# Performance work log

Measured on AMD Instinct MI355X. Metric: run time of the kernel, lower is better.

## Reference

```python
import jax, jax.numpy as jnp
import numpy as np
from jax import lax

ORDER = 2  # diffusion order per support, as in __init__(order=2)


def setup_inputs() -> dict:
    key = jax.random.key(0)
    k1, k2, k3 = jax.random.split(key, 3)
    N, C, V, L = 64, 32, 512, 13
    S, Kt, C_out = 3, 3, 32
    C_cat = (ORDER * S + 1) * C  # 224
    x = jax.random.normal(k1, (N, C, V, L), dtype=jnp.float32)
    support = jax.random.uniform(k2, (S, V, V), dtype=jnp.float32)
    # Conv2d(c_in=224, c_out=32, kernel=(1,Kt)) weights, PyTorch OIHW layout
    W = jax.random.normal(k3, (C_out, C_cat, 1, Kt), dtype=jnp.float32) * 0.02
    b = jnp.zeros((C_out,), dtype=jnp.float32)
    return {"x": x, "support": support, "W": W, "b": b}


def _nconv(x, A):
    # torch: A = A.T; einsum('ncvl,vw->ncwl', x, A.T)
    # => out[n,c,w,l] = sum_v A[w,v] * x[n,c,v,l]
    return jnp.einsum('ncvl,wv->ncwl', x, A)


def reference(x, support, W, b):
    out = [x]
    for s in range(support.shape[0]):  # small fixed support_len=3
        A = support[s]
        x1 = _nconv(x, A)
        out.append(x1)
        for _ in range(2, ORDER + 1):
            x1 = _nconv(x1, A)
            out.append(x1)
    h = jnp.concatenate(out, axis=1)  # [N, (order*S+1)*C, V, L]
    # Conv2d kernel (1, Kt), no padding, stride 1 -> temporal conv
    y = lax.conv_general_dilated(
        h, W, window_strides=(1, 1), padding='VALID',
        dimension_numbers=('NCHW', 'OIHW', 'NCHW'))
    y = y + b[None, :, None, None]
    # dropout is identity in eval mode
    return y
```

## Files before the change

### kernel.cpp

```cpp
#include <hip/hip_runtime.h>

typedef __attribute__((ext_vector_type(4))) float f32x4;
typedef __attribute__((ext_vector_type(8))) __bf16 bf16x8;
typedef __attribute__((ext_vector_type(4))) __bf16 bf16x4;
typedef __attribute__((ext_vector_type(4))) int i32x4;

#define SXE (26624 * 512)

__global__ __launch_bounds__(256)
void prep_x(const float* __restrict__ x, __bf16* __restrict__ Xv2) {
  const int vt = blockIdx.x, n = blockIdx.y, tid = threadIdx.x;
  __shared__ float Xs[32 * 209];
  const float* src = x + ((size_t)n * 32) * 6656 + vt * 16 * 13;
  for (int i = tid; i < 32 * 208; i += 256) {
    const int c = i / 208, r = i - c * 208;
    Xs[c * 209 + r] = src[(size_t)c * 6656 + r];
  }
  __syncthreads();
  for (int j = tid; j < 416; j += 256) {
    const int c = j & 31, l = j >> 5;
    bf16x8 o8[2];
    #pragma unroll
    for (int v = 0; v < 16; ++v) o8[v >> 3][v & 7] = (__bf16)Xs[c * 209 + v * 13 + l];
    __bf16* d = Xv2 + (((size_t)n * 13 + l) * 32 + c) * 512 + vt * 16;
    *(bf16x8*)d = o8[0];
    *(bf16x8*)(d + 8) = o8[1];
  }
}

__global__ __launch_bounds__(256)
void cast_A(const float* __restrict__ A, __bf16* __restrict__ Ab) {
  const int i = blockIdx.x * 256 + threadIdx.x;
  const float4 f = ((const float4*)A)[i];
  bf16x4 o;
  o[0] = (__bf16)f.x; o[1] = (__bf16)f.y; o[2] = (__bf16)f.z; o[3] = (__bf16)f.w;
  ((bf16x4*)Ab)[i] = o;
}

__global__ __launch_bounds__(256)
void gemm_bf16(const __bf16* __restrict__ Ab, const __bf16* __restrict__ SRC,
               __bf16* __restrict__ DSTB, size_t srcStride, size_t dstStride) {
  const int tid = threadIdx.x;
  const int lane = tid & 63, wave = tid >> 6, q = lane >> 4;
  const int bx = blockIdx.x, by = blockIdx.y, s = blockIdx.z;

  const __bf16* Amat = Ab + (size_t)s * 512 * 512;
  const __bf16* B = SRC + (size_t)s * srcStride;
  __bf16* D = DSTB + (size_t)s * dstStride;

  const int W0 = by * 128, B0 = bx * 128;
  const int wm = wave >> 1, wn = wave & 1;

  __shared__ __bf16 As[128 * 64];
  __shared__ __bf16 Bs[128 * 64];

  f32x4 acc[4][4];
  #pragma unroll
  for (int m = 0; m < 4; ++m)
    #pragma unroll
    for (int n = 0; n < 4; ++n) acc[m][n] = {0.f, 0.f, 0.f, 0.f};

  const int srow = lane >> 3, spos = lane & 7;

  for (int kt = 0; kt < 8; ++kt) {
    const int k0 = kt * 64;
    #pragma unroll
    for (int i = 0; i < 4; ++i) {
      const int slot = i * 4 + wave;
      const int r = slot * 8 + srow;
      const int gc = spos ^ (r & 7);
      const __bf16* ga = Amat + (size_t)(W0 + r) * 512 + k0 + gc * 8;
      const __bf16* gb = B    + (size_t)(B0 + r) * 512 + k0 + gc * 8;
      char* la = (char*)As + slot * 1024 + lane * 16;
      char* lb = (char*)Bs + slot * 1024 + lane * 16;
      __builtin_amdgcn_global_load_lds((const __attribute__((address_space(1))) unsigned int*)ga,
                                       (__attribute__((address_space(3))) unsigned int*)la, 16, 0, 0);
      __builtin_amdgcn_global_load_lds((const __attribute__((address_space(1))) unsigned int*)gb,
                                       (__attribute__((address_space(3))) unsigned int*)lb, 16, 0, 0);
    }
    __syncthreads();
    #pragma unroll
    for (int ks = 0; ks < 2; ++ks) {
      bf16x8 af[4], df[4];
      const int ch = ks * 4 + q;
      #pragma unroll
      for (int m = 0; m < 4; ++m) {
        const int r = wm * 64 + m * 16 + (lane & 15);
        af[m] = *(const bf16x8*)((const char*)As + r * 128 + ((ch ^ (r & 7)) << 4));
      }
      #pragma unroll
      for (int n = 0; n < 4; ++n) {
        const int r = wn * 64 + n * 16 + (lane & 15);
        df[n] = *(const bf16x8*)((const char*)Bs + r * 128 + ((ch ^ (r & 7)) << 4));
      }
      #pragma unroll
      for (int m = 0; m < 4; ++m)
        #pragma unroll
        for (int n = 0; n < 4; ++n)
          acc[m][n] = __builtin_amdgcn_mfma_f32_16x16x32_bf16(af[m], df[n], acc[m][n], 0, 0, 0);
    }
    __syncthreads();
  }

  #pragma unroll
  for (int m = 0; m < 4; ++m) {
    const int w = W0 + wm * 64 + m * 16 + q * 4;
    #pragma unroll
    for (int n = 0; n < 4; ++n) {
      const int b = B0 + wn * 64 + n * 16 + (lane & 15);
      bf16x4 o4;
      o4[0] = (__bf16)acc[m][n][0]; o4[1] = (__bf16)acc[m][n][1];
      o4[2] = (__bf16)acc[m][n][2]; o4[3] = (__bf16)acc[m][n][3];
      *(bf16x4*)(D + (size_t)b * 512 + w) = o4;
    }
  }
}

__global__ __launch_bounds__(256)
void conv_kernel(const __bf16* __restrict__ Xv2, const __bf16* __restrict__ Y1,
                 const __bf16* __restrict__ Y2, const float* __restrict__ W,
                 const float* __restrict__ bias, float* __restrict__ y) {
  const int vt = blockIdx.x;
  const int n  = blockIdx.y;
  const int tid = threadIdx.x;
  const int lane = tid & 63, wave = tid >> 6, q = lane >> 4, r16 = lane & 15;

  __shared__ char sm[59392];
  char* Ws = sm + 53248;

  const __bf16* gsrc[7] = {Xv2, Y1, Y2, Y1 + (size_t)SXE, Y2 + (size_t)SXE,
                           Y1 + 2 * (size_t)SXE, Y2 + 2 * (size_t)SXE};

  f32x4 acc[11][2];
  #pragma unroll
  for (int t = 0; t < 11; ++t) { acc[t][0] = {0,0,0,0}; acc[t][1] = {0,0,0,0}; }

  for (int g = 0; g < 7; ++g) {
    __syncthreads();
    const __bf16* src = gsrc[g] + ((size_t)n * 416) * 512 + vt * 64;
    #pragma unroll
    for (int it = 0; it < 13; ++it) {
      const int idx = it * 256 + tid;
      const int l = idx >> 8, rem = idx & 255, c = rem >> 3, h = rem & 7;
      i32x4 val = *(const i32x4*)(src + ((size_t)(l * 32 + c) << 9) + h * 8);
      *(i32x4*)(sm + l * 4096 + c * 128 + h * 16) = val;
    }
    for (int idx = tid; idx < 768; idx += 256) {
      const int f = idx >> 7, rem2 = idx & 127, lw = rem2 >> 1, half = rem2 & 1;
      const int kt = f >> 1, of = f & 1;
      const int o = of * 16 + (lw & 15);
      const int cc = g * 32 + (lw >> 4) * 8 + half * 4;
      bf16x4 w4;
      #pragma unroll
      for (int j = 0; j < 4; ++j)
        w4[j] = (__bf16)W[((size_t)o * 224 + cc + j) * 3 + kt];
      *(bf16x4*)(Ws + idx * 8) = w4;
    }
    __syncthreads();

    bf16x8 a8[13];
    const int gbase = q * 8 * 128 + (wave * 16 + r16) * 2;
    #pragma unroll
    for (int l = 0; l < 13; ++l) {
      bf16x8 a;
      #pragma unroll
      for (int j = 0; j < 8; ++j)
        a[j] = *(const __bf16*)(sm + l * 4096 + gbase + j * 128);
      a8[l] = a;
    }
    bf16x8 wf[6];
    #pragma unroll
    for (int f = 0; f < 6; ++f)
      wf[f] = *(const bf16x8*)(Ws + (f * 64 + lane) * 16);

    #pragma unroll
    for (int kt = 0; kt < 3; ++kt)
      #pragma unroll
      for (int of = 0; of < 2; ++of)
        #pragma unroll
        for (int t = 0; t < 11; ++t)
          acc[t][of] = __builtin_amdgcn_mfma_f32_16x16x32_bf16(a8[t + kt], wf[kt * 2 + of], acc[t][of], 0, 0, 0);
  }

  float* Ds = (float*)sm;
  const int o16 = lane & 15;
  for (int p = 0; p < 2; ++p) {
    __syncthreads();
    #pragma unroll
    for (int t = 0; t < 11; ++t) {
      const int vbase = wave * 16 + q * 4;
      #pragma unroll
      for (int rg = 0; rg < 4; ++rg)
        Ds[o16 * 708 + (vbase + rg) * 11 + t] = acc[t][p][rg];
    }
    __syncthreads();
    for (int i = 0; i < 11; ++i) {
      const int cg = tid + i * 256;
      const int oo = cg / 176, ch = cg - oo * 176;
      f32x4 v4 = *(const f32x4*)(Ds + oo * 708 + ch * 4);
      const float bo = bias[p * 16 + oo];
      v4[0] += bo; v4[1] += bo; v4[2] += bo; v4[3] += bo;
      float* yp = y + (((size_t)n * 32 + p * 16 + oo) * 512 + vt * 64) * 11 + ch * 4;
      *(f32x4*)yp = v4;
    }
  }
}

extern "C" void kernel_launch(void* const* d_in, const int* in_sizes, int n_in,
                              void* d_out, int out_size, void* d_ws, size_t ws_size,
                              hipStream_t stream) {
  (void)in_sizes; (void)n_in; (void)out_size; (void)ws_size;
  const float* x = (const float*)d_in[0];
  const float* A = (const float*)d_in[1];
  const float* W = (const float*)d_in[2];
  const float* b = (const float*)d_in[3];
  float* y = (float*)d_out;

  char* ws = (char*)d_ws;
  const size_t SXB = (size_t)SXE * 2;
  __bf16* Xv2 = (__bf16*)ws;
  __bf16* Y1  = (__bf16*)(ws + SXB);
  __bf16* Y2  = (__bf16*)(ws + 4 * SXB);
  __bf16* Ab  = (__bf16*)(ws + 7 * SXB);

  cast_A<<<dim3(768), 256, 0, stream>>>(A, Ab);
  prep_x<<<dim3(32, 64), 256, 0, stream>>>(x, Xv2);
  gemm_bf16<<<dim3(208, 4, 3), 256, 0, stream>>>(Ab, Xv2, Y1, 0, (size_t)SXE);
  gemm_bf16<<<dim3(208, 4, 3), 256, 0, stream>>>(Ab, Y1, Y2, (size_t)SXE, (size_t)SXE);
  conv_kernel<<<dim3(8, 64), 256, 0, stream>>>(Xv2, Y1, Y2, W, b, y);
}
```

Baseline: 235.6 us.

## Widen GEMM tile to 256x128 and remap blocks for XCD-aware locality

The diffusion GEMM tile grows from 128x128 to 256 rows of A by 128 columns, so each wave holds a 4x8 accumulator array and every B tile loaded from global memory is reused twice as much. The launch becomes a flat 1D grid with a block index remap that spreads consecutive logical tiles across the 8 XCDs, so tiles sharing the same B columns and support land on the same XCD and can share its L2. The change raises register pressure and LDS use to 48KB, which may lower occupancy, and halves the block count.

```diff
diff --git a/kernel.cpp b/kernel.cpp
--- a/kernel.cpp
+++ b/kernel.cpp
@@ -39,75 +39,80 @@
 
 __global__ __launch_bounds__(256)
 void gemm_bf16(const __bf16* __restrict__ Ab, const __bf16* __restrict__ SRC,
-               __bf16* __restrict__ DSTB, size_t srcStride, size_t dstStride) {
+               __bf16* __restrict__ DSTB, size_t srcStride, size_t dstStride, int cpx) {
   const int tid = threadIdx.x;
-  const int lane = tid & 63, wave = tid >> 6, q = lane >> 4;
-  const int bx = blockIdx.x, by = blockIdx.y, s = blockIdx.z;
+  const int lane = tid & 63, wave = tid >> 6, q = lane >> 4, r16 = lane & 15;
+
+  const int bid = blockIdx.x;
+  const int lg = (bid & 7) * cpx + (bid >> 3);
+  const int bx = lg / 6, r6 = lg % 6, s = r6 >> 1, by = r6 & 1;
 
   const __bf16* Amat = Ab + (size_t)s * 512 * 512;
   const __bf16* B = SRC + (size_t)s * srcStride;
   __bf16* D = DSTB + (size_t)s * dstStride;
 
-  const int W0 = by * 128, B0 = bx * 128;
+  const int W0 = by * 256, B0 = bx * 128;
   const int wm = wave >> 1, wn = wave & 1;
 
-  __shared__ __bf16 As[128 * 64];
-  __shared__ __bf16 Bs[128 * 64];
-
-  f32x4 acc[4][4];
+  __shared__ char gsm[49152];
+  char* As = gsm;
+  char* Bs = gsm + 32768;
+
+  f32x4 acc[4][8];
   #pragma unroll
   for (int m = 0; m < 4; ++m)
     #pragma unroll
-    for (int n = 0; n < 4; ++n) acc[m][n] = {0.f, 0.f, 0.f, 0.f};
+    for (int n = 0; n < 8; ++n) acc[m][n] = {0.f, 0.f, 0.f, 0.f};
 
   const int srow = lane >> 3, spos = lane & 7;
 
   for (int kt = 0; kt < 8; ++kt) {
     const int k0 = kt * 64;
     #pragma unroll
-    for (int i = 0; i < 4; ++i) {
+    for (int i = 0; i < 12; ++i) {
       const int slot = i * 4 + wave;
-      const int r = slot * 8 + srow;
-      const int gc = spos ^ (r & 7);
-      const __bf16* ga = Amat + (size_t)(W0 + r) * 512 + k0 + gc * 8;
-      const __bf16* gb = B    + (size_t)(B0 + r) * 512 + k0 + gc * 8;
-      char* la = (char*)As + slot * 1024 + lane * 16;
-      char* lb = (char*)Bs + slot * 1024 + lane * 16;
-      __builtin_amdgcn_global_load_lds((const __attribute__((address_space(1))) unsigned int*)ga,
-                                       (__attribute__((address_space(3))) unsigned int*)la, 16, 0, 0);
-      __builtin_amdgcn_global_load_lds((const __attribute__((address_space(1))) unsigned int*)gb,
-                                       (__attribute__((address_space(3))) unsigned int*)lb, 16, 0, 0);
+      const int rr = (slot & 31 & ~32) ;
+      (void)rr;
+      const int gc = spos ^ (((slot & 31) * 0 + (slot < 32 ? (slot * 8 + srow) : ((slot - 32) * 8 + srow))) & 7);
+      const int row = (slot < 32) ? (slot * 8 + srow) : ((slot - 32) * 8 + srow);
+      const __bf16* g = (slot < 32)
+          ? Amat + (size_t)(W0 + row) * 512 + k0 + ((spos ^ (row & 7)) * 8)
+          : B    + (size_t)(B0 + row) * 512 + k0 + ((spos ^ (row & 7)) * 8);
+      (void)gc;
+      char* ld = gsm + slot * 1024 + lane * 16;
+      __builtin_amdgcn_global_load_lds((const __attribute__((address_space(1))) unsigned int*)g,
+                                       (__attribute__((address_space(3))) unsigned int*)ld, 16, 0, 0);
     }
     __syncthreads();
     #pragma unroll
     for (int ks = 0; ks < 2; ++ks) {
-      bf16x8 af[4], df[4];
+      bf16x8 af[8], df[4];
       const int ch = ks * 4 + q;
       #pragma unroll
+      for (int n = 0; n < 8; ++n) {
+        const int r = wn * 128 + n * 16 + r16;
+        af[n] = *(const bf16x8*)(As + r * 128 + ((ch ^ (r & 7)) << 4));
+      }
+      #pragma unroll
       for (int m = 0; m < 4; ++m) {
-        const int r = wm * 64 + m * 16 + (lane & 15);
-        af[m] = *(const bf16x8*)((const char*)As + r * 128 + ((ch ^ (r & 7)) << 4));
-      }
-      #pragma unroll
-      for (int n = 0; n < 4; ++n) {
-        const int r = wn * 64 + n * 16 + (lane & 15);
-        df[n] = *(const bf16x8*)((const char*)Bs + r * 128 + ((ch ^ (r & 7)) << 4));
+        const int r = wm * 64 + m * 16 + r16;
+        df[m] = *(const bf16x8*)(Bs + r * 128 + ((ch ^ (r & 7)) << 4));
       }
       #pragma unroll
       for (int m = 0; m < 4; ++m)
         #pragma unroll
-        for (int n = 0; n < 4; ++n)
-          acc[m][n] = __builtin_amdgcn_mfma_f32_16x16x32_bf16(af[m], df[n], acc[m][n], 0, 0, 0);
+        for (int n = 0; n < 8; ++n)
+          acc[m][n] = __builtin_amdgcn_mfma_f32_16x16x32_bf16(af[n], df[m], acc[m][n], 0, 0, 0);
     }
     __syncthreads();
   }
 
   #pragma unroll
   for (int m = 0; m < 4; ++m) {
-    const int w = W0 + wm * 64 + m * 16 + q * 4;
-    #pragma unroll
-    for (int n = 0; n < 4; ++n) {
-      const int b = B0 + wn * 64 + n * 16 + (lane & 15);
+    const int b = B0 + wm * 64 + m * 16 + r16;
+    #pragma unroll
+    for (int n = 0; n < 8; ++n) {
+      const int w = W0 + wn * 128 + n * 16 + q * 4;
       bf16x4 o4;
       o4[0] = (__bf16)acc[m][n][0]; o4[1] = (__bf16)acc[m][n][1];
       o4[2] = (__bf16)acc[m][n][2]; o4[3] = (__bf16)acc[m][n][3];
@@ -225,7 +230,7 @@
 
   cast_A<<<dim3(768), 256, 0, stream>>>(A, Ab);
   prep_x<<<dim3(32, 64), 256, 0, stream>>>(x, Xv2);
-  gemm_bf16<<<dim3(208, 4, 3), 256, 0, stream>>>(Ab, Xv2, Y1, 0, (size_t)SXE);
-  gemm_bf16<<<dim3(208, 4, 3), 256, 0, stream>>>(Ab, Y1, Y2, (size_t)SXE, (size_t)SXE);
+  gemm_bf16<<<dim3(1248), 256, 0, stream>>>(Ab, Xv2, Y1, 0, (size_t)SXE, 156);
+  gemm_bf16<<<dim3(1248), 256, 0, stream>>>(Ab, Y1, Y2, (size_t)SXE, (size_t)SXE, 156);
   conv_kernel<<<dim3(8, 64), 256, 0, stream>>>(Xv2, Y1, Y2, W, b, y);
 }
```

New measurement: 270.6 us. 14.9% more time.
